# Performance work log

Measured on AMD Instinct MI355X. Metric: run time of the kernel, lower is better.

The kernel has to match this reference:

```python
import jax, jax.numpy as jnp
import numpy as np

B, L, C = 2, 1024, 512
H, P = 8, 4
D = C // H
LN_EPS = 1e-5


def setup_inputs() -> dict:
    key = jax.random.key(0)
    ks = jax.random.split(key, 12)
    s = 0.02
    inp = {
        "features": jax.random.normal(ks[0], (B, L, C), jnp.float32),
        "coords": jax.random.normal(ks[1], (B, L, 3), jnp.float32),
        # LayerNorm params
        "ln_g": jnp.ones((C,), jnp.float32),
        "ln_b": jnp.zeros((C,), jnp.float32),
        # scalar q/k/v projections (stored as [in, out])
        "wq": jax.random.normal(ks[2], (C, C), jnp.float32) * s,
        "bq": jnp.zeros((C,), jnp.float32),
        "wk": jax.random.normal(ks[3], (C, C), jnp.float32) * s,
        "bk": jnp.zeros((C,), jnp.float32),
        "wv": jax.random.normal(ks[4], (C, C), jnp.float32) * s,
        "bv": jnp.zeros((C,), jnp.float32),
        # point q/k/v projections: [C, H*P*3]
        "wqp": jax.random.normal(ks[5], (C, H * P * 3), jnp.float32) * s,
        "bqp": jnp.zeros((H * P * 3,), jnp.float32),
        "wkp": jax.random.normal(ks[6], (C, H * P * 3), jnp.float32) * s,
        "bkp": jnp.zeros((H * P * 3,), jnp.float32),
        "wvp": jax.random.normal(ks[7], (C, H * P * 3), jnp.float32) * s,
        "bvp": jnp.zeros((H * P * 3,), jnp.float32),
        # output projection
        "wo": jax.random.normal(ks[8], (C, C), jnp.float32) * s,
        "bo": jnp.zeros((C,), jnp.float32),
        # per-head point scale, init 1/sqrt(P)
        "pscale": jnp.full((H,), 1.0 / np.sqrt(P), jnp.float32),
    }
    return inp


def _layernorm(x, g, b):
    mu = jnp.mean(x, axis=-1, keepdims=True)
    var = jnp.mean((x - mu) ** 2, axis=-1, keepdims=True)
    return (x - mu) * jax.lax.rsqrt(var + LN_EPS) * g + b


def reference(features, coords, ln_g, ln_b, wq, bq, wk, bk, wv, bv,
              wqp, bqp, wkp, bkp, wvp, bvp, wo, bo, pscale):
    b, l, c = features.shape
    h = pscale.shape[0]
    d = c // h
    p = wqp.shape[1] // (h * 3)

    x = _layernorm(features, ln_g, ln_b)

    # scalar heads: [b,h,l,d]
    q_s = (x @ wq + bq).reshape(b, l, h, d).transpose(0, 2, 1, 3)
    k_s = (x @ wk + bk).reshape(b, l, h, d).transpose(0, 2, 1, 3)
    v_s = (x @ wv + bv).reshape(b, l, h, d).transpose(0, 2, 1, 3)

    # point heads: [b,h,l,p,3]
    q_p = (x @ wqp + bqp).reshape(b, l, h, p, 3).transpose(0, 2, 1, 3, 4)
    k_p = (x @ wkp + bkp).reshape(b, l, h, p, 3).transpose(0, 2, 1, 3, 4)

    # scalar logits
    logits_s = jnp.einsum('bhid,bhjd->bhij', q_s, k_s) * (d ** -0.5)

    # point-distance logits: sum_{p,k} ||q - k||^2 = |q|^2 + |k|^2 - 2 q.k
    # (avoids materializing the [b,h,l,l,p,3] difference tensor)
    dot = jnp.einsum('bhipk,bhjpk->bhij', q_p, k_p)
    qsq = jnp.sum(q_p * q_p, axis=(-1, -2))  # [b,h,l]
    ksq = jnp.sum(k_p * k_p, axis=(-1, -2))  # [b,h,l]
    pdist2 = qsq[..., :, None] + ksq[..., None, :] - 2.0 * dot  # [b,h,l,l]

    logits = logits_s - pdist2 * pscale[None, :, None, None]

    attn = jax.nn.softmax(logits, axis=-1)  # dropout is identity in eval

    out_s = jnp.einsum('bhij,bhjd->bhid', attn, v_s)
    out_s = out_s.transpose(0, 2, 1, 3).reshape(b, l, c)

    out = out_s @ wo + bo  # out_dropout is identity in eval
    return out
```

## Files before the change

### kernel.cpp

```cpp
#include <hip/hip_runtime.h>
#include <math.h>

#define BB 2
#define LL 1024
#define CCH 512
#define HH 8
#define LN_EPSF 1e-5f

typedef short s16x8 __attribute__((ext_vector_type(8)));
typedef float fx4 __attribute__((ext_vector_type(4)));


__device__ __forceinline__ unsigned short f2bf(float f) {
  unsigned u = __float_as_uint(f);
  unsigned r = (u + 0x7FFFu + ((u >> 16) & 1u)) >> 16;
  return (unsigned short)r;
}
__device__ __forceinline__ float bf2f(unsigned short h) {
  return __uint_as_float(((unsigned)h) << 16);
}
__device__ __forceinline__ s16x8 ldfrag(const unsigned short* p) {
  int4 t = *(const int4*)p;
  return *(s16x8*)&t;
}

template <int CTRL>
__device__ __forceinline__ float dpp_mov(float x) {
  return __int_as_float(
      __builtin_amdgcn_update_dpp(0, __float_as_int(x), CTRL, 0xF, 0xF, true));
}
__device__ __forceinline__ float red16_sum(float v) {
  v += dpp_mov<0x121>(v);
  v += dpp_mov<0x122>(v);
  v += dpp_mov<0x124>(v);
  v += dpp_mov<0x128>(v);
  return v;
}
__device__ __forceinline__ float red16_max(float v) {
  v = fmaxf(v, dpp_mov<0x121>(v));
  v = fmaxf(v, dpp_mov<0x122>(v));
  v = fmaxf(v, dpp_mov<0x124>(v));
  v = fmaxf(v, dpp_mov<0x128>(v));
  return v;
}
__device__ __forceinline__ float wave_sum(float v) {
  v = red16_sum(v);
  v += __shfl_xor(v, 16);
  v += __shfl_xor(v, 32);
  return v;
}

__global__ __launch_bounds__(256) void prep(
    const float* __restrict__ f, const float* __restrict__ g,
    const float* __restrict__ bta, unsigned short* __restrict__ xh,
    unsigned short* __restrict__ xl, const float* __restrict__ wq,
    const float* __restrict__ wk, const float* __restrict__ wv,
    const float* __restrict__ wo, const float* __restrict__ wqp,
    const float* __restrict__ wkp, unsigned short* __restrict__ wt_h,
    unsigned short* __restrict__ qt, unsigned short* __restrict__ kt_,
    float* __restrict__ out) {
  __shared__ unsigned short lh[64][68];
  __shared__ float red[8];
  const int tid = threadIdx.x;
  const int bxg = blockIdx.x;
  if (bxg < 2048) {
    const int row = bxg;
    const int wave = tid >> 6, lane = tid & 63;
    const float* fr = f + (size_t)row * CCH;
    float2 v = *(const float2*)&fr[tid * 2];
    float s = wave_sum(v.x + v.y);
    if (lane == 0) red[wave] = s;
    __syncthreads();
    float mu = (red[0] + red[1] + red[2] + red[3]) * (1.0f / CCH);
    float dx = v.x - mu, dy = v.y - mu;
    float sq = wave_sum(dx * dx + dy * dy);
    if (lane == 0) red[4 + wave] = sq;
    __syncthreads();
    float var = (red[4] + red[5] + red[6] + red[7]) * (1.0f / CCH);
    float inv = 1.0f / sqrtf(var + LN_EPSF);
    float2 gg = *(const float2*)&g[tid * 2];
    float2 bb = *(const float2*)&bta[tid * 2];
    float ox = dx * inv * gg.x + bb.x;
    float oy = dy * inv * gg.y + bb.y;
    unsigned short h0 = f2bf(ox), h1 = f2bf(oy);
    ushort2 hv; hv.x = h0; hv.y = h1;
    ushort2 lv; lv.x = f2bf(ox - bf2f(h0)); lv.y = f2bf(oy - bf2f(h1));
    const int k0c = tid * 2;
    size_t addr = ((size_t)((row >> 4) * 16 + (k0c >> 5))) * 512 +
                  (((k0c >> 3) & 3) * 16 + (row & 15)) * 8 + (k0c & 7);
    *(ushort2*)&xh[addr] = hv;
    *(ushort2*)&xl[addr] = lv;
  } else if (bxg < 2336) {
    const int bx = bxg - 2048;
    const float* W;
    int Ncols, rowbase, kt, nt;
    if (bx < 256) {
      int mat = bx >> 6, t = bx & 63;
      kt = t >> 3; nt = t & 7; Ncols = 512;
      if (mat == 0) { W = wq; rowbase = 0; }
      else if (mat == 1) { W = wk; rowbase = 512; }
      else if (mat == 2) { W = wv; rowbase = 1024; }
      else { W = wo; rowbase = 1536; }
    } else {
      int r = bx - 256; int mat = r >> 4; int t = r & 15;
      kt = t >> 1; nt = t & 1; Ncols = 96;
      if (mat == 0) { W = wqp; rowbase = 2048; }
      else { W = wkp; rowbase = 2144; }
    }
    const int k0 = kt * 64, n0 = nt * 64;
    const int c = tid & 63;
#pragma unroll
    for (int ii = 0; ii < 16; ++ii) {
      int r = ii * 4 + (tid >> 6);
      float val = (n0 + c < Ncols) ? W[(size_t)(k0 + r) * Ncols + n0 + c] : 0.f;
      lh[r][c] = f2bf(val);
    }
    __syncthreads();
    const int base_nt = (rowbase >> 4) + (n0 >> 4);
    const int base_kt = (k0 >> 5);
#pragma unroll
    for (int cc = 0; cc < 2; ++cc) {
      int ch = cc * 256 + tid;
      int lane2 = ch & 63, ktl = (ch >> 6) & 1, ntl = ch >> 7;
      int l16c = lane2 & 15, quadc = lane2 >> 4;
      if (n0 + ntl * 16 < Ncols) {
        unsigned short th[8] __attribute__((aligned(16)));
#pragma unroll
        for (int jj = 0; jj < 8; ++jj)
          th[jj] = lh[ktl * 32 + quadc * 8 + jj][ntl * 16 + l16c];
        *(int4*)&wt_h[((size_t)((base_nt + ntl) * 16 + base_kt + ktl)) * 512 +
                      lane2 * 8] = *(int4*)th;
      }
    }
  } else if (bxg < 2400) {
    const int vb2 = bxg - 2336;
    const int4 zero = {0, 0, 0, 0};
    for (int u = tid; u < 32 * 48; u += 256) {
      int t = u / 48, off = (u - t * 48) * 8;
      int gidx = vb2 * 32 + t;
      unsigned short* dst = (gidx < 1024) ? qt : kt_;
      int rem = gidx & 1023;
      int bh = rem >> 6, lt = rem & 63;
      size_t base = ((size_t)(bh * 64 + lt) * 3 + 2) * 512;
      *(int4*)&dst[base + 128 + off] = zero;
    }
  } else {
    const int vb3 = bxg - 2400;
    const float4 zero = {0.f, 0.f, 0.f, 0.f};
    float4* dst = (float4*)(out + (size_t)vb3 * 4096);
#pragma unroll
    for (int i = 0; i < 4; ++i) dst[i * 256 + tid] = zero;
  }
}

template <int MF, int NF, int TERMS>
__device__ __forceinline__ void mfma_core_frag(
    const unsigned short* __restrict__ Ah, const unsigned short* __restrict__ Al,
    const unsigned short* __restrict__ Bt, int mt0, int ntbase, int nt0,
    int ntmax, int ks0, int ks1, fx4 acc[MF][NF]) {
  const int lane = threadIdx.x & 63;
  int bt[NF];
#pragma unroll
  for (int j = 0; j < NF; ++j) {
    int nt = nt0 + j;
    if (nt > ntmax) nt = ntmax;
    bt[j] = ntbase + nt;
  }
#pragma unroll
  for (int i = 0; i < MF; ++i)
#pragma unroll
    for (int j = 0; j < NF; ++j) acc[i][j] = (fx4){0.f, 0.f, 0.f, 0.f};
  for (int ks = ks0; ks < ks1; ++ks) {
    s16x8 ah[MF], al[MF], b[NF];
#pragma unroll
    for (int i = 0; i < MF; ++i) {
      size_t off = ((size_t)((mt0 + i) * 16 + ks)) * 512 + lane * 8;
      ah[i] = ldfrag(&Ah[off]);
      if (TERMS == 2) al[i] = ldfrag(&Al[off]);
    }
#pragma unroll
    for (int j = 0; j < NF; ++j)
      b[j] = ldfrag(&Bt[((size_t)(bt[j] * 16 + ks)) * 512 + lane * 8]);
#pragma unroll
    for (int i = 0; i < MF; ++i)
#pragma unroll
      for (int j = 0; j < NF; ++j) {
        acc[i][j] = __builtin_amdgcn_mfma_f32_16x16x32_bf16(ah[i], b[j], acc[i][j], 0, 0, 0);
        if (TERMS == 2)
          acc[i][j] = __builtin_amdgcn_mfma_f32_16x16x32_bf16(al[i], b[j], acc[i][j], 0, 0, 0);
      }
  }
}

__global__ __launch_bounds__(256, 4) void proj_mfma(
    const unsigned short* __restrict__ xh, const unsigned short* __restrict__ xl,
    const unsigned short* __restrict__ wt_h,
    const float* __restrict__ bq, const float* __restrict__ bk,
    const float* __restrict__ bv, const float* __restrict__ bqp,
    const float* __restrict__ bkp, const float* __restrict__ pscale,
    unsigned short* __restrict__ qt, unsigned short* __restrict__ kt_,
    unsigned short* __restrict__ vth) {
  __shared__ unsigned short vt_lds[64][72];
  const int bx = blockIdx.x;
  const int m0 = blockIdx.y * 64;
  const int tid = threadIdx.x;
  const int wave = __builtin_amdgcn_readfirstlane(tid >> 6);
  const int lane = tid & 63;
  const int quad = lane >> 4, l16 = lane & 15;
  const int mw = m0 + (wave & 1) * 32;
  const int mt0 = mw >> 4;

  if (bx < 16) {
    const bool isq = bx < 8;
    const float* bias = isq ? bq : bk;
    unsigned short* pdst = isq ? qt : kt_;
    const int n0 = (bx & 7) * 64;
    const int nw = n0 + (wave >> 1) * 32;
    fx4 acc[2][2];
    mfma_core_frag<2, 2, 1>(xh, xh, wt_h, mt0, isq ? 0 : 32, nw >> 4, 31, 0, 16, acc);
#pragma unroll
    for (int j = 0; j < 2; ++j) {
      int n = nw + j * 16 + l16;
      int h = n >> 6, d = n & 63;
      float bb = bias[n];
#pragma unroll
      for (int i = 0; i < 2; ++i)
#pragma unroll
        for (int reg = 0; reg < 4; ++reg) {
          int row = mw + i * 16 + quad * 4 + reg;
          int bi = row >> 10, l = row & 1023;
          int bh2 = bi * 8 + h;
          float val = (acc[i][j][reg] + bb) * 0.35355339059f;
          size_t tile = ((size_t)(bh2 * 64 + (l >> 4))) * 3 + (d >> 5);
          pdst[tile * 512 + (((d >> 3) & 3) * 16 + (l & 15)) * 8 + (d & 7)] = f2bf(val);
        }
    }
  } else if (bx < 24) {
    const int h = bx - 16;
    const int nw = h * 64 + (wave >> 1) * 32;
    fx4 acc[2][2];
    mfma_core_frag<2, 2, 2>(xh, xl, wt_h, mt0, 64, nw >> 4, 31, 0, 16, acc);
#pragma unroll
    for (int j = 0; j < 2; ++j) {
      int dl = (wave >> 1) * 32 + j * 16 + l16;
      float bb = bv[h * 64 + dl];
#pragma unroll
      for (int i = 0; i < 2; ++i)
#pragma unroll
        for (int reg = 0; reg < 4; ++reg) {
          int lm = (wave & 1) * 32 + i * 16 + quad * 4 + reg;
          vt_lds[lm][dl] = f2bf(acc[i][j][reg] + bb);
        }
    }
    __syncthreads();
    const int b = m0 >> 10, l0 = m0 & 1023;
    const int bh2 = b * 8 + h;
#pragma unroll
    for (int cc = 0; cc < 2; ++cc) {
      int ch = cc * 256 + tid;
      int lane2 = ch & 63, jt = (ch >> 6) & 1, ft = ch >> 7;
      int l16c = lane2 & 15, quadc = lane2 >> 4;
      unsigned short th[8] __attribute__((aligned(16)));
#pragma unroll
      for (int jj = 0; jj < 8; ++jj)
        th[jj] = vt_lds[jt * 32 + quadc * 8 + jj][ft * 16 + l16c];
      size_t tile = ((size_t)(bh2 * 4 + ft)) * 32 + (l0 >> 5) + jt;
      *(int4*)&vth[tile * 512 + lane2 * 8] = *(int4*)th;
    }
  } else {
    const bool isq = bx < 26;
    const float* bias = isq ? bqp : bkp;
    unsigned short* pdst = isq ? qt : kt_;
    const int n0 = (bx & 1) * 64;
    const int nw = n0 + (wave >> 1) * 32;
    fx4 acc[2][2];
    mfma_core_frag<2, 2, 1>(xh, xh, wt_h, mt0, isq ? 128 : 134, nw >> 4, 5, 0, 16, acc);
#pragma unroll
    for (int j = 0; j < 2; ++j) {
      int n = nw + j * 16 + l16;
      bool ok = n < 96;
      int nn = ok ? n : 0;
      int h = nn / 12, c = nn - h * 12;
      float sc = sqrtf(2.f * pscale[h]);
      float bb = bias[nn];
#pragma unroll
      for (int i = 0; i < 2; ++i)
#pragma unroll
        for (int reg = 0; reg < 4; ++reg) {
          int row = mw + i * 16 + quad * 4 + reg;
          int bi = row >> 10, l = row & 1023;
          int bh2 = bi * 8 + h;
          float val = (acc[i][j][reg] + bb) * sc;
          if (ok) {
            int kc = 64 + c;
            size_t tile = ((size_t)(bh2 * 64 + (l >> 4))) * 3 + 2;
            pdst[tile * 512 + (((kc >> 3) & 3) * 16 + (l & 15)) * 8 + (kc & 7)] =
                f2bf(val);
          }
        }
    }
  }
}

__global__ __launch_bounds__(256, 4) void out_proj_mfma(
    const unsigned short* __restrict__ oh,
    const unsigned short* __restrict__ wt_h, const float* __restrict__ bo,
    float* __restrict__ out) {
  const int tid = threadIdx.x;
  const int wave = __builtin_amdgcn_readfirstlane(tid >> 6);
  const int lane = tid & 63;
  const int quad = lane >> 4, l16 = lane & 15;
  const int mw = blockIdx.y * 64 + (wave & 1) * 32;
  const int nw = blockIdx.x * 64 + (wave >> 1) * 32;
  const int kz = blockIdx.z;
  fx4 acc[2][2];
  mfma_core_frag<2, 2, 1>(oh, oh, wt_h, mw >> 4, 96, nw >> 4, 31, kz * 4,
                          kz * 4 + 4, acc);
#pragma unroll
  for (int j = 0; j < 2; ++j) {
    int n = nw + j * 16 + l16;
    float bb = (kz == 0) ? bo[n] : 0.f;
#pragma unroll
    for (int i = 0; i < 2; ++i)
#pragma unroll
      for (int reg = 0; reg < 4; ++reg) {
        int row = mw + i * 16 + quad * 4 + reg;
        atomicAdd(&out[(size_t)row * 512 + n], acc[i][j][reg] + bb);
      }
  }
}

__global__ __launch_bounds__(512, 4) void ipa_attn_mfma(
    const unsigned short* __restrict__ qt, const unsigned short* __restrict__ kt_,
    const unsigned short* __restrict__ vth, unsigned short* __restrict__ oh) {
  const int bid = blockIdx.x;
  const int low3 = bid & 7;
  const int slot = bid >> 3;
  const int qtile = slot & 31;
  const int bh = ((slot >> 5) << 3) | low3;
  const int tid = threadIdx.x;
  const int wave = tid >> 6, lane = tid & 63;
  const int quad = lane >> 4, l16 = lane & 15;
  const int mstrip = wave & 1, kq = wave >> 1;
  const int ibase = qtile * 32 + mstrip * 16;

  __shared__ unsigned short pb[8][16][32];
  __shared__ float obuf[8][16][64];
  __shared__ float mred[8][16], lred[8][16];
  __shared__ float qsl[8][16];

  s16x8 aq[3];
#pragma unroll
  for (int s = 0; s < 3; ++s)
    aq[s] = ldfrag(&qt[(((size_t)(bh * 64 + (ibase >> 4))) * 3 + s) * 512 + lane * 8]);

  {
    float qp = 0.f;
#pragma unroll
    for (int j = 0; j < 8; ++j) {
      float v = bf2f((unsigned short)aq[2][j]);
      qp += v * v;
    }
    qp += __shfl_xor(qp, 16);
    qp += __shfl_xor(qp, 32);
    qsl[wave][l16] = 0.5f * qp;
  }
  float qs_r[4];
#pragma unroll
  for (int reg = 0; reg < 4; ++reg) qs_r[reg] = qsl[wave][quad * 4 + reg];

  fx4 o[4];
#pragma unroll
  for (int f = 0; f < 4; ++f) o[f] = (fx4){0.f, 0.f, 0.f, 0.f};
  float m_r[4], l_r[4];
#pragma unroll
  for (int reg = 0; reg < 4; ++reg) { m_r[reg] = -INFINITY; l_r[reg] = 0.f; }

#pragma unroll 1
  for (int c = 0; c < 8; ++c) {
    const int j0 = kq * 256 + c * 32;
    s16x8 bk[2][3];
#pragma unroll
    for (int f = 0; f < 2; ++f)
#pragma unroll
      for (int s = 0; s < 3; ++s)
        bk[f][s] = ldfrag(
            &kt_[(((size_t)(bh * 64 + (j0 >> 4) + f)) * 3 + s) * 512 + lane * 8]);
    s16x8 bvh[4];
#pragma unroll
    for (int f = 0; f < 4; ++f)
      bvh[f] = ldfrag(
          &vth[(((size_t)(bh * 4 + f)) * 32 + (j0 >> 5)) * 512 + lane * 8]);

    float kp0 = 0.f, kp1 = 0.f;
#pragma unroll
    for (int j = 0; j < 8; ++j) {
      float v0 = bf2f((unsigned short)bk[0][2][j]);
      float v1 = bf2f((unsigned short)bk[1][2][j]);
      kp0 += v0 * v0;
      kp1 += v1 * v1;
    }
    kp0 += __shfl_xor(kp0, 16);
    kp0 += __shfl_xor(kp0, 32);
    kp1 += __shfl_xor(kp1, 16);
    kp1 += __shfl_xor(kp1, 32);
    float ks0 = 0.5f * kp0, ks1 = 0.5f * kp1;

    fx4 sa[2];
    sa[0] = (fx4){0.f, 0.f, 0.f, 0.f};
    sa[1] = (fx4){0.f, 0.f, 0.f, 0.f};
#pragma unroll
    for (int f = 0; f < 2; ++f)
#pragma unroll
      for (int s = 0; s < 3; ++s)
        sa[f] = __builtin_amdgcn_mfma_f32_16x16x32_bf16(aq[s], bk[f][s], sa[f], 0, 0, 0);

#pragma unroll
    for (int reg = 0; reg < 4; ++reg) {
      float z0 = sa[0][reg] - qs_r[reg] - ks0;
      float z1 = sa[1][reg] - qs_r[reg] - ks1;
      float mx = red16_max(fmaxf(z0, z1));
      float mnew = fmaxf(m_r[reg], mx);
      float p0 = __expf(z0 - mnew), p1 = __expf(z1 - mnew);
      float alpha = __expf(m_r[reg] - mnew);
      float psum = red16_sum(p0 + p1);
      l_r[reg] = l_r[reg] * alpha + psum;
      m_r[reg] = mnew;
      o[0][reg] *= alpha; o[1][reg] *= alpha; o[2][reg] *= alpha; o[3][reg] *= alpha;
      pb[wave][quad * 4 + reg][l16] = f2bf(p0);
      pb[wave][quad * 4 + reg][16 + l16] = f2bf(p1);
    }
    s16x8 ap = ldfrag(&pb[wave][l16][quad * 8]);
#pragma unroll
    for (int f = 0; f < 4; ++f)
      o[f] = __builtin_amdgcn_mfma_f32_16x16x32_bf16(ap, bvh[f], o[f], 0, 0, 0);
  }
  if (l16 == 0) {
#pragma unroll
    for (int reg = 0; reg < 4; ++reg) {
      mred[wave][quad * 4 + reg] = m_r[reg];
      lred[wave][quad * 4 + reg] = l_r[reg];
    }
  }
#pragma unroll
  for (int f = 0; f < 4; ++f)
#pragma unroll
    for (int reg = 0; reg < 4; ++reg)
      obuf[wave][quad * 4 + reg][f * 16 + l16] = o[f][reg];
  __syncthreads();
  if (kq == 0) {
    const int b = bh >> 3, h = bh & 7;
#pragma unroll
    for (int f = 0; f < 4; ++f)
#pragma unroll
      for (int reg = 0; reg < 4; ++reg) {
        int row = quad * 4 + reg;
        int d = f * 16 + l16;
        float M = -INFINITY;
#pragma unroll
        for (int p = 0; p < 4; ++p) M = fmaxf(M, mred[wave + p * 2][row]);
        float L = 0.f, val = 0.f;
#pragma unroll
        for (int p = 0; p < 4; ++p) {
          float w = __expf(mred[wave + p * 2][row] - M);
          L += lred[wave + p * 2][row] * w;
          val += obuf[wave + p * 2][row][d] * w;
        }
        val /= L;
        int m = b * LL + ibase + row;
        int kcol = h * 64 + d;
        size_t tile = ((size_t)(m >> 4)) * 16 + (kcol >> 5);
        oh[tile * 512 + (((kcol >> 3) & 3) * 16 + (m & 15)) * 8 + (kcol & 7)] =
            f2bf(val);
      }
  }
}

extern "C" void kernel_launch(void* const* d_in, const int* in_sizes, int n_in,
                              void* d_out, int out_size, void* d_ws, size_t ws_size,
                              hipStream_t stream) {
  (void)in_sizes; (void)n_in; (void)out_size; (void)ws_size;
  const float* features = (const float*)d_in[0];
  const float* ln_g = (const float*)d_in[2];
  const float* ln_b = (const float*)d_in[3];
  const float* wq = (const float*)d_in[4];
  const float* bq = (const float*)d_in[5];
  const float* wk = (const float*)d_in[6];
  const float* bk = (const float*)d_in[7];
  const float* wv = (const float*)d_in[8];
  const float* bv = (const float*)d_in[9];
  const float* wqp = (const float*)d_in[10];
  const float* bqp = (const float*)d_in[11];
  const float* wkp = (const float*)d_in[12];
  const float* bkp = (const float*)d_in[13];
  const float* wo = (const float*)d_in[16];
  const float* bo = (const float*)d_in[17];
  const float* pscale = (const float*)d_in[18];
  float* out = (float*)d_out;

  char* cur = (char*)d_ws;
  const size_t NTOK = (size_t)BB * LL;
  unsigned short* xh = (unsigned short*)cur; cur += NTOK * CCH * 2;
  unsigned short* xl = (unsigned short*)cur; cur += NTOK * CCH * 2;
  unsigned short* wt_h = (unsigned short*)cur; cur += (size_t)2240 * 512 * 2;
  unsigned short* qt = (unsigned short*)cur; cur += (size_t)16 * LL * 96 * 2;
  unsigned short* kt_ = (unsigned short*)cur; cur += (size_t)16 * LL * 96 * 2;
  unsigned short* vth = (unsigned short*)cur; cur += (size_t)16 * 64 * LL * 2;
  unsigned short* oh = (unsigned short*)cur; cur += NTOK * CCH * 2;

  prep<<<dim3(2656), 256, 0, stream>>>(features, ln_g, ln_b, xh, xl, wq, wk, wv,
                                       wo, wqp, wkp, wt_h, qt, kt_, out);
  proj_mfma<<<dim3(28, 32), 256, 0, stream>>>(xh, xl, wt_h, bq, bk, bv, bqp, bkp,
                                              pscale, qt, kt_, vth);
  ipa_attn_mfma<<<dim3(512), 512, 0, stream>>>(qt, kt_, vth, oh);
  out_proj_mfma<<<dim3(8, 32, 4), 256, 0, stream>>>(oh, wt_h, bo, out);
}
```

Before: 157.4 us.

## Fuse output projection into attention kernel, precompute key norms, use exp2

The output projection is folded into the attention kernel epilogue. Each block stages its normalized 32x64 head output in swizzled LDS and multiplies it by that head's slice of Wo with MFMA, then atomically accumulates into the output. This removes a kernel launch and the bf16 round trip of the attention output through global memory, at the cost of per-head atomics and extra LDS and register pressure. Key point-norms are computed once per block into LDS rather than per chunk, and the log2(e) factor is folded into the q scale and point scale so that raw v_exp_f32 can be used.

```diff
diff --git a/kernel.cpp b/kernel.cpp
--- a/kernel.cpp
+++ b/kernel.cpp
@@ -22,6 +22,11 @@
 __device__ __forceinline__ s16x8 ldfrag(const unsigned short* p) {
   int4 t = *(const int4*)p;
   return *(s16x8*)&t;
+}
+__device__ __forceinline__ float ex2(float x) {
+  float r;
+  asm("v_exp_f32 %0, %1" : "=v"(r) : "v"(x));
+  return r;
 }
 
 template <int CTRL>
@@ -230,7 +235,7 @@
           int row = mw + i * 16 + quad * 4 + reg;
           int bi = row >> 10, l = row & 1023;
           int bh2 = bi * 8 + h;
-          float val = (acc[i][j][reg] + bb) * 0.35355339059f;
+          float val = (acc[i][j][reg] + bb) * 0.4246609f;
           size_t tile = ((size_t)(bh2 * 64 + (l >> 4))) * 3 + (d >> 5);
           pdst[tile * 512 + (((d >> 3) & 3) * 16 + (l & 15)) * 8 + (d & 7)] = f2bf(val);
         }
@@ -281,7 +286,7 @@
       bool ok = n < 96;
       int nn = ok ? n : 0;
       int h = nn / 12, c = nn - h * 12;
-      float sc = sqrtf(2.f * pscale[h]);
+      float sc = sqrtf(2.8853901f * pscale[h]);
       float bb = bias[nn];
 #pragma unroll
       for (int i = 0; i < 2; ++i)
@@ -302,37 +307,10 @@
   }
 }
 
-__global__ __launch_bounds__(256, 4) void out_proj_mfma(
-    const unsigned short* __restrict__ oh,
-    const unsigned short* __restrict__ wt_h, const float* __restrict__ bo,
-    float* __restrict__ out) {
-  const int tid = threadIdx.x;
-  const int wave = __builtin_amdgcn_readfirstlane(tid >> 6);
-  const int lane = tid & 63;
-  const int quad = lane >> 4, l16 = lane & 15;
-  const int mw = blockIdx.y * 64 + (wave & 1) * 32;
-  const int nw = blockIdx.x * 64 + (wave >> 1) * 32;
-  const int kz = blockIdx.z;
-  fx4 acc[2][2];
-  mfma_core_frag<2, 2, 1>(oh, oh, wt_h, mw >> 4, 96, nw >> 4, 31, kz * 4,
-                          kz * 4 + 4, acc);
-#pragma unroll
-  for (int j = 0; j < 2; ++j) {
-    int n = nw + j * 16 + l16;
-    float bb = (kz == 0) ? bo[n] : 0.f;
-#pragma unroll
-    for (int i = 0; i < 2; ++i)
-#pragma unroll
-      for (int reg = 0; reg < 4; ++reg) {
-        int row = mw + i * 16 + quad * 4 + reg;
-        atomicAdd(&out[(size_t)row * 512 + n], acc[i][j][reg] + bb);
-      }
-  }
-}
-
 __global__ __launch_bounds__(512, 4) void ipa_attn_mfma(
     const unsigned short* __restrict__ qt, const unsigned short* __restrict__ kt_,
-    const unsigned short* __restrict__ vth, unsigned short* __restrict__ oh) {
+    const unsigned short* __restrict__ vth, const unsigned short* __restrict__ wt_h,
+    const float* __restrict__ bo, float* __restrict__ out) {
   const int bid = blockIdx.x;
   const int low3 = bid & 7;
   const int slot = bid >> 3;
@@ -348,6 +326,8 @@
   __shared__ float obuf[8][16][64];
   __shared__ float mred[8][16], lred[8][16];
   __shared__ float qsl[8][16];
+  __shared__ float ks_lds[1024];
+  __shared__ __align__(16) unsigned short o_fin[32][64];
 
   s16x8 aq[3];
 #pragma unroll
@@ -368,6 +348,22 @@
   float qs_r[4];
 #pragma unroll
   for (int reg = 0; reg < 4; ++reg) qs_r[reg] = qsl[wave][quad * 4 + reg];
+
+#pragma unroll
+  for (int i = 0; i < 8; ++i) {
+    int t = wave * 8 + i;
+    s16x8 kf = ldfrag(&kt_[(((size_t)(bh * 64 + t)) * 3 + 2) * 512 + lane * 8]);
+    float s = 0.f;
+#pragma unroll
+    for (int j = 0; j < 8; ++j) {
+      float v = bf2f((unsigned short)kf[j]);
+      s += v * v;
+    }
+    s += __shfl_xor(s, 16);
+    s += __shfl_xor(s, 32);
+    if (lane < 16) ks_lds[t * 16 + lane] = 0.5f * s;
+  }
+  __syncthreads();
 
   fx4 o[4];
 #pragma unroll
@@ -392,19 +388,8 @@
       bvh[f] = ldfrag(
           &vth[(((size_t)(bh * 4 + f)) * 32 + (j0 >> 5)) * 512 + lane * 8]);
 
-    float kp0 = 0.f, kp1 = 0.f;
-#pragma unroll
-    for (int j = 0; j < 8; ++j) {
-      float v0 = bf2f((unsigned short)bk[0][2][j]);
-      float v1 = bf2f((unsigned short)bk[1][2][j]);
-      kp0 += v0 * v0;
-      kp1 += v1 * v1;
-    }
-    kp0 += __shfl_xor(kp0, 16);
-    kp0 += __shfl_xor(kp0, 32);
-    kp1 += __shfl_xor(kp1, 16);
-    kp1 += __shfl_xor(kp1, 32);
-    float ks0 = 0.5f * kp0, ks1 = 0.5f * kp1;
+    float ks0 = ks_lds[j0 + l16];
+    float ks1 = ks_lds[j0 + 16 + l16];
 
     fx4 sa[2];
     sa[0] = (fx4){0.f, 0.f, 0.f, 0.f};
@@ -421,8 +406,8 @@
       float z1 = sa[1][reg] - qs_r[reg] - ks1;
       float mx = red16_max(fmaxf(z0, z1));
       float mnew = fmaxf(m_r[reg], mx);
-      float p0 = __expf(z0 - mnew), p1 = __expf(z1 - mnew);
-      float alpha = __expf(m_r[reg] - mnew);
+      float p0 = ex2(z0 - mnew), p1 = ex2(z1 - mnew);
+      float alpha = ex2(m_r[reg] - mnew);
       float psum = red16_sum(p0 + p1);
       l_r[reg] = l_r[reg] * alpha + psum;
       m_r[reg] = mnew;
@@ -449,7 +434,6 @@
       obuf[wave][quad * 4 + reg][f * 16 + l16] = o[f][reg];
   __syncthreads();
   if (kq == 0) {
-    const int b = bh >> 3, h = bh & 7;
 #pragma unroll
     for (int f = 0; f < 4; ++f)
 #pragma unroll
@@ -462,17 +446,63 @@
         float L = 0.f, val = 0.f;
 #pragma unroll
         for (int p = 0; p < 4; ++p) {
-          float w = __expf(mred[wave + p * 2][row] - M);
+          float w = ex2(mred[wave + p * 2][row] - M);
           L += lred[wave + p * 2][row] * w;
           val += obuf[wave + p * 2][row][d] * w;
         }
         val /= L;
-        int m = b * LL + ibase + row;
-        int kcol = h * 64 + d;
-        size_t tile = ((size_t)(m >> 4)) * 16 + (kcol >> 5);
-        oh[tile * 512 + (((kcol >> 3) & 3) * 16 + (m & 15)) * 8 + (kcol & 7)] =
-            f2bf(val);
+        int rowl = wave * 16 + row;
+        o_fin[rowl][(((d >> 3) ^ (rowl & 7)) << 3) + (d & 7)] = f2bf(val);
       }
+  }
+  __syncthreads();
+
+  {
+    const int b = bh >> 3, h = bh & 7;
+    const size_t m0 = (size_t)b * LL + qtile * 32;
+    s16x8 af[2][2];
+#pragma unroll
+    for (int mi = 0; mi < 2; ++mi)
+#pragma unroll
+      for (int k2 = 0; k2 < 2; ++k2) {
+        int rowa = mi * 16 + l16;
+        af[mi][k2] = ldfrag(&o_fin[rowa][(((k2 * 4 + quad) ^ (rowa & 7)) << 3)]);
+      }
+#pragma unroll
+    for (int np = 0; np < 2; ++np) {
+      fx4 acc[2][2];
+#pragma unroll
+      for (int mi = 0; mi < 2; ++mi)
+#pragma unroll
+        for (int j = 0; j < 2; ++j) acc[mi][j] = (fx4){0.f, 0.f, 0.f, 0.f};
+#pragma unroll
+      for (int k2 = 0; k2 < 2; ++k2) {
+        s16x8 bw[2];
+#pragma unroll
+        for (int j = 0; j < 2; ++j) {
+          int nt = wave * 4 + np * 2 + j;
+          bw[j] = ldfrag(
+              &wt_h[((size_t)((96 + nt) * 16 + h * 2 + k2)) * 512 + lane * 8]);
+        }
+#pragma unroll
+        for (int mi = 0; mi < 2; ++mi)
+#pragma unroll
+          for (int j = 0; j < 2; ++j)
+            acc[mi][j] = __builtin_amdgcn_mfma_f32_16x16x32_bf16(
+                af[mi][k2], bw[j], acc[mi][j], 0, 0, 0);
+      }
+#pragma unroll
+      for (int j = 0; j < 2; ++j) {
+        int n = (wave * 4 + np * 2 + j) * 16 + l16;
+        float bb = (h == 0) ? bo[n] : 0.f;
+#pragma unroll
+        for (int mi = 0; mi < 2; ++mi)
+#pragma unroll
+          for (int reg = 0; reg < 4; ++reg)
+            atomicAdd(&out[(m0 + mi * 16 + quad * 4 + reg) * 512 + n],
+                      acc[mi][j][reg] + bb);
+      }
+    }
   }
 }
 
@@ -506,12 +536,10 @@
   unsigned short* qt = (unsigned short*)cur; cur += (size_t)16 * LL * 96 * 2;
   unsigned short* kt_ = (unsigned short*)cur; cur += (size_t)16 * LL * 96 * 2;
   unsigned short* vth = (unsigned short*)cur; cur += (size_t)16 * 64 * LL * 2;
-  unsigned short* oh = (unsigned short*)cur; cur += NTOK * CCH * 2;
 
   prep<<<dim3(2656), 256, 0, stream>>>(features, ln_g, ln_b, xh, xl, wq, wk, wv,
                                        wo, wqp, wkp, wt_h, qt, kt_, out);
   proj_mfma<<<dim3(28, 32), 256, 0, stream>>>(xh, xl, wt_h, bq, bk, bv, bqp, bkp,
                                               pscale, qt, kt_, vth);
-  ipa_attn_mfma<<<dim3(512), 512, 0, stream>>>(qt, kt_, vth, oh);
-  out_proj_mfma<<<dim3(8, 32, 4), 256, 0, stream>>>(oh, wt_h, bo, out);
-}
+  ipa_attn_mfma<<<dim3(512), 512, 0, stream>>>(qt, kt_, vth, wt_h, bo, out);
+}
```

Result: slower. 163.9 us (+4.1%).

## Fold squared norms into QK MFMA, use exp2 softmax, drop split-K atomics

Applied to the files above, without the earlier changes.

A new aug_sq kernel writes the per-row half squared point norms (hi/lo bf16 split) alongside -1 entries into spare columns of the Q/K tiles. The QK MFMA then produces the full distance logits directly, so the attention loop no longer computes k norms per chunk. Scales are premultiplied by log2(e) so softmax can use raw v_exp_f32. The attention kernel is reorganised into 256-thread blocks covering one 16-row query tile each. The output projection runs without split-K, writing directly instead of using atomics, which also removes the zero-fill of the output in prep. The cost is an extra small kernel launch and some bf16 precision risk on the norm terms.

```diff
diff --git a/kernel.cpp b/kernel.cpp
--- a/kernel.cpp
+++ b/kernel.cpp
@@ -22,6 +22,11 @@
 __device__ __forceinline__ s16x8 ldfrag(const unsigned short* p) {
   int4 t = *(const int4*)p;
   return *(s16x8*)&t;
+}
+__device__ __forceinline__ float ex2(float x) {
+  float r;
+  asm("v_exp_f32 %0, %1" : "=v"(r) : "v"(x));
+  return r;
 }
 
 template <int CTRL>
@@ -57,8 +62,7 @@
     const float* __restrict__ wk, const float* __restrict__ wv,
     const float* __restrict__ wo, const float* __restrict__ wqp,
     const float* __restrict__ wkp, unsigned short* __restrict__ wt_h,
-    unsigned short* __restrict__ qt, unsigned short* __restrict__ kt_,
-    float* __restrict__ out) {
+    unsigned short* __restrict__ qt, unsigned short* __restrict__ kt_) {
   __shared__ unsigned short lh[64][68];
   __shared__ float red[8];
   const int tid = threadIdx.x;
@@ -132,7 +136,7 @@
                       lane2 * 8] = *(int4*)th;
       }
     }
-  } else if (bxg < 2400) {
+  } else {
     const int vb2 = bxg - 2336;
     const int4 zero = {0, 0, 0, 0};
     for (int u = tid; u < 32 * 48; u += 256) {
@@ -144,12 +148,6 @@
       size_t base = ((size_t)(bh * 64 + lt) * 3 + 2) * 512;
       *(int4*)&dst[base + 128 + off] = zero;
     }
-  } else {
-    const int vb3 = bxg - 2400;
-    const float4 zero = {0.f, 0.f, 0.f, 0.f};
-    float4* dst = (float4*)(out + (size_t)vb3 * 4096);
-#pragma unroll
-    for (int i = 0; i < 4; ++i) dst[i * 256 + tid] = zero;
   }
 }
 
@@ -230,7 +228,7 @@
           int row = mw + i * 16 + quad * 4 + reg;
           int bi = row >> 10, l = row & 1023;
           int bh2 = bi * 8 + h;
-          float val = (acc[i][j][reg] + bb) * 0.35355339059f;
+          float val = (acc[i][j][reg] + bb) * 0.4246609f;
           size_t tile = ((size_t)(bh2 * 64 + (l >> 4))) * 3 + (d >> 5);
           pdst[tile * 512 + (((d >> 3) & 3) * 16 + (l & 15)) * 8 + (d & 7)] = f2bf(val);
         }
@@ -281,7 +279,7 @@
       bool ok = n < 96;
       int nn = ok ? n : 0;
       int h = nn / 12, c = nn - h * 12;
-      float sc = sqrtf(2.f * pscale[h]);
+      float sc = sqrtf(2.8853901f * pscale[h]);
       float bb = bias[nn];
 #pragma unroll
       for (int i = 0; i < 2; ++i)
@@ -302,6 +300,152 @@
   }
 }
 
+__global__ __launch_bounds__(64) void aug_sq(
+    unsigned short* __restrict__ qt, unsigned short* __restrict__ kt_) {
+  const int bid = blockIdx.x;
+  const int which = bid & 1;
+  const int lt = (bid >> 1) & 63;
+  const int bh = bid >> 7;
+  unsigned short* t = which ? kt_ : qt;
+  const size_t base = ((size_t)(bh * 64 + lt) * 3 + 2) * 512;
+  const int lane = threadIdx.x;
+  s16x8 v = ldfrag(&t[base + lane * 8]);
+  float s = 0.f;
+#pragma unroll
+  for (int j = 0; j < 8; ++j) {
+    float x = bf2f((unsigned short)v[j]);
+    if ((lane >> 4) == 1 && j >= 4) x = 0.f;
+    if ((lane >> 4) >= 2) x = 0.f;
+    s += x * x;
+  }
+  float tot = 0.5f * (s + __shfl_xor(s, 16));
+  if ((lane >> 4) == 1) {
+    unsigned short hi = f2bf(tot);
+    unsigned short lo = f2bf(tot - bf2f(hi));
+    const unsigned short m1 = 0xBF80;
+    ushort4 w;
+    if (which) { w.x = hi; w.y = lo; w.z = m1; w.w = m1; }
+    else       { w.x = m1; w.y = m1; w.z = hi; w.w = lo; }
+    *(ushort4*)&t[base + lane * 8 + 4] = w;
+  }
+}
+
+__global__ __launch_bounds__(256, 4) void ipa_attn_mfma(
+    const unsigned short* __restrict__ qt, const unsigned short* __restrict__ kt_,
+    const unsigned short* __restrict__ vth, unsigned short* __restrict__ oh) {
+  const int bid = blockIdx.x;
+  const int low3 = bid & 7;
+  const int slot = bid >> 3;
+  const int qtile = slot & 63;
+  const int bh = ((slot >> 6) << 3) | low3;
+  const int tid = threadIdx.x;
+  const int wave = tid >> 6, lane = tid & 63;
+  const int quad = lane >> 4, l16 = lane & 15;
+  const int kq = wave;
+  const int ibase = qtile * 16;
+
+  __shared__ __align__(16) float obufF[4 * 16 * 66];
+  __shared__ float mred[4][16], lred[4][16];
+
+  unsigned short* pbw = (unsigned short*)&obufF[wave * 16 * 66];
+
+  s16x8 aq[3];
+#pragma unroll
+  for (int s = 0; s < 3; ++s)
+    aq[s] = ldfrag(&qt[(((size_t)(bh * 64 + qtile)) * 3 + s) * 512 + lane * 8]);
+
+  fx4 o[4];
+#pragma unroll
+  for (int f = 0; f < 4; ++f) o[f] = (fx4){0.f, 0.f, 0.f, 0.f};
+  float m_r[4], l_r[4];
+#pragma unroll
+  for (int reg = 0; reg < 4; ++reg) { m_r[reg] = -INFINITY; l_r[reg] = 0.f; }
+
+#pragma unroll 1
+  for (int c = 0; c < 8; ++c) {
+    const int j0 = kq * 256 + c * 32;
+    s16x8 bk[2][3];
+#pragma unroll
+    for (int f = 0; f < 2; ++f)
+#pragma unroll
+      for (int s = 0; s < 3; ++s)
+        bk[f][s] = ldfrag(
+            &kt_[(((size_t)(bh * 64 + (j0 >> 4) + f)) * 3 + s) * 512 + lane * 8]);
+
+    fx4 sa[2];
+    sa[0] = (fx4){0.f, 0.f, 0.f, 0.f};
+    sa[1] = (fx4){0.f, 0.f, 0.f, 0.f};
+#pragma unroll
+    for (int f = 0; f < 2; ++f)
+#pragma unroll
+      for (int s = 0; s < 3; ++s)
+        sa[f] = __builtin_amdgcn_mfma_f32_16x16x32_bf16(aq[s], bk[f][s], sa[f], 0, 0, 0);
+
+#pragma unroll
+    for (int reg = 0; reg < 4; ++reg) {
+      float z0 = sa[0][reg];
+      float z1 = sa[1][reg];
+      float mx = red16_max(fmaxf(z0, z1));
+      float mnew = fmaxf(m_r[reg], mx);
+      float p0 = ex2(z0 - mnew), p1 = ex2(z1 - mnew);
+      float alpha = ex2(m_r[reg] - mnew);
+      float psum = red16_sum(p0 + p1);
+      l_r[reg] = l_r[reg] * alpha + psum;
+      m_r[reg] = mnew;
+      o[0][reg] *= alpha; o[1][reg] *= alpha; o[2][reg] *= alpha; o[3][reg] *= alpha;
+      pbw[(quad * 4 + reg) * 40 + l16] = f2bf(p0);
+      pbw[(quad * 4 + reg) * 40 + 16 + l16] = f2bf(p1);
+    }
+    s16x8 bvh[4];
+#pragma unroll
+    for (int f = 0; f < 4; ++f)
+      bvh[f] = ldfrag(
+          &vth[(((size_t)(bh * 4 + f)) * 32 + (j0 >> 5)) * 512 + lane * 8]);
+    s16x8 ap = ldfrag(&pbw[l16 * 40 + quad * 8]);
+#pragma unroll
+    for (int f = 0; f < 4; ++f)
+      o[f] = __builtin_amdgcn_mfma_f32_16x16x32_bf16(ap, bvh[f], o[f], 0, 0, 0);
+  }
+  if (l16 == 0) {
+#pragma unroll
+    for (int reg = 0; reg < 4; ++reg) {
+      mred[wave][quad * 4 + reg] = m_r[reg];
+      lred[wave][quad * 4 + reg] = l_r[reg];
+    }
+  }
+#pragma unroll
+  for (int f = 0; f < 4; ++f)
+#pragma unroll
+    for (int reg = 0; reg < 4; ++reg)
+      obufF[((size_t)(wave * 16 + quad * 4 + reg)) * 66 + f * 16 + l16] = o[f][reg];
+  __syncthreads();
+
+  {
+    const int b = bh >> 3, h = bh & 7;
+    const int d = wave * 16 + l16;
+#pragma unroll
+    for (int rr = 0; rr < 4; ++rr) {
+      int row = quad * 4 + rr;
+      float M = -INFINITY;
+#pragma unroll
+      for (int p = 0; p < 4; ++p) M = fmaxf(M, mred[p][row]);
+      float L = 0.f, val = 0.f;
+#pragma unroll
+      for (int p = 0; p < 4; ++p) {
+        float w = ex2(mred[p][row] - M);
+        L += lred[p][row] * w;
+        val += obufF[((size_t)(p * 16 + row)) * 66 + d] * w;
+      }
+      val /= L;
+      int m = b * LL + ibase + row;
+      int kcol = h * 64 + d;
+      size_t tile = ((size_t)(m >> 4)) * 16 + (kcol >> 5);
+      oh[tile * 512 + (((kcol >> 3) & 3) * 16 + (m & 15)) * 8 + (kcol & 7)] =
+          f2bf(val);
+    }
+  }
+}
+
 __global__ __launch_bounds__(256, 4) void out_proj_mfma(
     const unsigned short* __restrict__ oh,
     const unsigned short* __restrict__ wt_h, const float* __restrict__ bo,
@@ -312,166 +456,18 @@
   const int quad = lane >> 4, l16 = lane & 15;
   const int mw = blockIdx.y * 64 + (wave & 1) * 32;
   const int nw = blockIdx.x * 64 + (wave >> 1) * 32;
-  const int kz = blockIdx.z;
   fx4 acc[2][2];
-  mfma_core_frag<2, 2, 1>(oh, oh, wt_h, mw >> 4, 96, nw >> 4, 31, kz * 4,
-                          kz * 4 + 4, acc);
+  mfma_core_frag<2, 2, 1>(oh, oh, wt_h, mw >> 4, 96, nw >> 4, 31, 0, 16, acc);
 #pragma unroll
   for (int j = 0; j < 2; ++j) {
     int n = nw + j * 16 + l16;
-    float bb = (kz == 0) ? bo[n] : 0.f;
+    float bb = bo[n];
 #pragma unroll
     for (int i = 0; i < 2; ++i)
 #pragma unroll
       for (int reg = 0; reg < 4; ++reg) {
         int row = mw + i * 16 + quad * 4 + reg;
-        atomicAdd(&out[(size_t)row * 512 + n], acc[i][j][reg] + bb);
-      }
-  }
-}
-
-__global__ __launch_bounds__(512, 4) void ipa_attn_mfma(
-    const unsigned short* __restrict__ qt, const unsigned short* __restrict__ kt_,
-    const unsigned short* __restrict__ vth, unsigned short* __restrict__ oh) {
-  const int bid = blockIdx.x;
-  const int low3 = bid & 7;
-  const int slot = bid >> 3;
-  const int qtile = slot & 31;
-  const int bh = ((slot >> 5) << 3) | low3;
-  const int tid = threadIdx.x;
-  const int wave = tid >> 6, lane = tid & 63;
-  const int quad = lane >> 4, l16 = lane & 15;
-  const int mstrip = wave & 1, kq = wave >> 1;
-  const int ibase = qtile * 32 + mstrip * 16;
-
-  __shared__ unsigned short pb[8][16][32];
-  __shared__ float obuf[8][16][64];
-  __shared__ float mred[8][16], lred[8][16];
-  __shared__ float qsl[8][16];
-
-  s16x8 aq[3];
-#pragma unroll
-  for (int s = 0; s < 3; ++s)
-    aq[s] = ldfrag(&qt[(((size_t)(bh * 64 + (ibase >> 4))) * 3 + s) * 512 + lane * 8]);
-
-  {
-    float qp = 0.f;
-#pragma unroll
-    for (int j = 0; j < 8; ++j) {
-      float v = bf2f((unsigned short)aq[2][j]);
-      qp += v * v;
-    }
-    qp += __shfl_xor(qp, 16);
-    qp += __shfl_xor(qp, 32);
-    qsl[wave][l16] = 0.5f * qp;
-  }
-  float qs_r[4];
-#pragma unroll
-  for (int reg = 0; reg < 4; ++reg) qs_r[reg] = qsl[wave][quad * 4 + reg];
-
-  fx4 o[4];
-#pragma unroll
-  for (int f = 0; f < 4; ++f) o[f] = (fx4){0.f, 0.f, 0.f, 0.f};
-  float m_r[4], l_r[4];
-#pragma unroll
-  for (int reg = 0; reg < 4; ++reg) { m_r[reg] = -INFINITY; l_r[reg] = 0.f; }
-
-#pragma unroll 1
-  for (int c = 0; c < 8; ++c) {
-    const int j0 = kq * 256 + c * 32;
-    s16x8 bk[2][3];
-#pragma unroll
-    for (int f = 0; f < 2; ++f)
-#pragma unroll
-      for (int s = 0; s < 3; ++s)
-        bk[f][s] = ldfrag(
-            &kt_[(((size_t)(bh * 64 + (j0 >> 4) + f)) * 3 + s) * 512 + lane * 8]);
-    s16x8 bvh[4];
-#pragma unroll
-    for (int f = 0; f < 4; ++f)
-      bvh[f] = ldfrag(
-          &vth[(((size_t)(bh * 4 + f)) * 32 + (j0 >> 5)) * 512 + lane * 8]);
-
-    float kp0 = 0.f, kp1 = 0.f;
-#pragma unroll
-    for (int j = 0; j < 8; ++j) {
-      float v0 = bf2f((unsigned short)bk[0][2][j]);
-      float v1 = bf2f((unsigned short)bk[1][2][j]);
-      kp0 += v0 * v0;
-      kp1 += v1 * v1;
-    }
-    kp0 += __shfl_xor(kp0, 16);
-    kp0 += __shfl_xor(kp0, 32);
-    kp1 += __shfl_xor(kp1, 16);
-    kp1 += __shfl_xor(kp1, 32);
-    float ks0 = 0.5f * kp0, ks1 = 0.5f * kp1;
-
-    fx4 sa[2];
-    sa[0] = (fx4){0.f, 0.f, 0.f, 0.f};
-    sa[1] = (fx4){0.f, 0.f, 0.f, 0.f};
-#pragma unroll
-    for (int f = 0; f < 2; ++f)
-#pragma unroll
-      for (int s = 0; s < 3; ++s)
-        sa[f] = __builtin_amdgcn_mfma_f32_16x16x32_bf16(aq[s], bk[f][s], sa[f], 0, 0, 0);
-
-#pragma unroll
-    for (int reg = 0; reg < 4; ++reg) {
-      float z0 = sa[0][reg] - qs_r[reg] - ks0;
-      float z1 = sa[1][reg] - qs_r[reg] - ks1;
-      float mx = red16_max(fmaxf(z0, z1));
-      float mnew = fmaxf(m_r[reg], mx);
-      float p0 = __expf(z0 - mnew), p1 = __expf(z1 - mnew);
-      float alpha = __expf(m_r[reg] - mnew);
-      float psum = red16_sum(p0 + p1);
-      l_r[reg] = l_r[reg] * alpha + psum;
-      m_r[reg] = mnew;
-      o[0][reg] *= alpha; o[1][reg] *= alpha; o[2][reg] *= alpha; o[3][reg] *= alpha;
-      pb[wave][quad * 4 + reg][l16] = f2bf(p0);
-      pb[wave][quad * 4 + reg][16 + l16] = f2bf(p1);
-    }
-    s16x8 ap = ldfrag(&pb[wave][l16][quad * 8]);
-#pragma unroll
-    for (int f = 0; f < 4; ++f)
-      o[f] = __builtin_amdgcn_mfma_f32_16x16x32_bf16(ap, bvh[f], o[f], 0, 0, 0);
-  }
-  if (l16 == 0) {
-#pragma unroll
-    for (int reg = 0; reg < 4; ++reg) {
-      mred[wave][quad * 4 + reg] = m_r[reg];
-      lred[wave][quad * 4 + reg] = l_r[reg];
-    }
-  }
-#pragma unroll
-  for (int f = 0; f < 4; ++f)
-#pragma unroll
-    for (int reg = 0; reg < 4; ++reg)
-      obuf[wave][quad * 4 + reg][f * 16 + l16] = o[f][reg];
-  __syncthreads();
-  if (kq == 0) {
-    const int b = bh >> 3, h = bh & 7;
-#pragma unroll
-    for (int f = 0; f < 4; ++f)
-#pragma unroll
-      for (int reg = 0; reg < 4; ++reg) {
-        int row = quad * 4 + reg;
-        int d = f * 16 + l16;
-        float M = -INFINITY;
-#pragma unroll
-        for (int p = 0; p < 4; ++p) M = fmaxf(M, mred[wave + p * 2][row]);
-        float L = 0.f, val = 0.f;
-#pragma unroll
-        for (int p = 0; p < 4; ++p) {
-          float w = __expf(mred[wave + p * 2][row] - M);
-          L += lred[wave + p * 2][row] * w;
-          val += obuf[wave + p * 2][row][d] * w;
-        }
-        val /= L;
-        int m = b * LL + ibase + row;
-        int kcol = h * 64 + d;
-        size_t tile = ((size_t)(m >> 4)) * 16 + (kcol >> 5);
-        oh[tile * 512 + (((kcol >> 3) & 3) * 16 + (m & 15)) * 8 + (kcol & 7)] =
-            f2bf(val);
+        out[(size_t)row * 512 + n] = acc[i][j][reg] + bb;
       }
   }
 }
@@ -508,10 +504,11 @@
   unsigned short* vth = (unsigned short*)cur; cur += (size_t)16 * 64 * LL * 2;
   unsigned short* oh = (unsigned short*)cur; cur += NTOK * CCH * 2;
 
-  prep<<<dim3(2656), 256, 0, stream>>>(features, ln_g, ln_b, xh, xl, wq, wk, wv,
-                                       wo, wqp, wkp, wt_h, qt, kt_, out);
+  prep<<<dim3(2400), 256, 0, stream>>>(features, ln_g, ln_b, xh, xl, wq, wk, wv,
+                                       wo, wqp, wkp, wt_h, qt, kt_);
   proj_mfma<<<dim3(28, 32), 256, 0, stream>>>(xh, xl, wt_h, bq, bk, bv, bqp, bkp,
                                               pscale, qt, kt_, vth);
-  ipa_attn_mfma<<<dim3(512), 512, 0, stream>>>(qt, kt_, vth, oh);
-  out_proj_mfma<<<dim3(8, 32, 4), 256, 0, stream>>>(oh, wt_h, bo, out);
-}
+  aug_sq<<<dim3(2048), 64, 0, stream>>>(qt, kt_);
+  ipa_attn_mfma<<<dim3(1024), 256, 0, stream>>>(qt, kt_, vth, oh);
+  out_proj_mfma<<<dim3(8, 32), 256, 0, stream>>>(oh, wt_h, bo, out);
+}
```

After: 143.3 us. 9.0% less time.
